# Kernel optimization log

Hardware: AMD Instinct MI355X
Metric: run time of the kernel (lower is better)

The kernel has to match this reference:

```python
import jax, jax.numpy as jnp
import numpy as np

K = 32
BN_EPS = 1e-5
GRID = [[0.1, 0.1, 0.1], [0.5, 0.5, 0.5], [0.2, 0.2, 0.05]]


def setup_inputs() -> dict:
    key = jax.random.key(0)
    ks = jax.random.split(key, 8)
    B, P, C = 4, 6144, 64
    N = B * P
    feat = jax.random.normal(ks[0], (N, C), jnp.float32)
    coord = jax.random.normal(ks[1], (N, 3), jnp.float32) * 10.0
    batch = jnp.repeat(jnp.arange(B, dtype=jnp.int32), P)
    # feature_judge params: Linear(C,64) -> BatchNorm1d(64, eval) -> ReLU -> Linear(64,3)
    W1 = jax.random.normal(ks[2], (C, 64), jnp.float32) / np.sqrt(C)
    b1 = jnp.zeros((64,), jnp.float32)
    gamma = jnp.ones((64,), jnp.float32)
    beta = jnp.zeros((64,), jnp.float32)
    bn_mean = jax.random.normal(ks[3], (64,), jnp.float32) * 0.1
    bn_var = jax.random.uniform(ks[4], (64,), jnp.float32, 0.5, 1.5)
    W2 = jax.random.normal(ks[5], (64, 3), jnp.float32) / 8.0
    b2 = jnp.zeros((3,), jnp.float32)
    return {"feat": feat, "coord": coord, "batch": batch, "W1": W1, "b1": b1,
            "gamma": gamma, "beta": beta, "bn_mean": bn_mean, "bn_var": bn_var,
            "W2": W2, "b2": b2}


def _geometry(coord, B):
    # coord: [N,3] with equal-size contiguous batches -> [B,P,3]
    N = coord.shape[0]
    P = N // B
    pts = coord.reshape(B, P, 3)
    sq = jnp.sum(pts * pts, axis=-1)                               # [B,P]
    d2 = sq[:, :, None] + sq[:, None, :] - 2.0 * jnp.einsum('bpd,bqd->bpq', pts, pts)
    dist = jnp.sqrt(jnp.maximum(d2, 1e-12))                        # [B,P,P]
    _, idx = jax.lax.top_k(-dist, K + 1)                           # smallest K+1
    idx = idx[:, :, 1:]                                            # drop self -> [B,P,K]
    nbrs = jax.vmap(lambda p, i: p[i])(pts, idx)                   # [B,P,K,3]
    centered = nbrs - nbrs.mean(axis=2, keepdims=True)
    cov = jnp.einsum('bpki,bpkj->bpij', centered, centered) / (K - 1)  # [B,P,3,3]
    ev = jnp.linalg.eigvalsh(cov)[..., ::-1]                       # descending, == svd S (PSD)
    ev = ev / jnp.sum(ev, axis=-1, keepdims=True)
    linearity = (ev[..., 0] - (ev[..., 1] + ev[..., 2])).reshape(N)
    nbr_d = jnp.take_along_axis(dist, idx, axis=2)                 # [B,P,K]
    density = (1.0 / (nbr_d.mean(axis=-1) + 1e-6)).reshape(N)
    return linearity, density


def reference(feat, coord, batch, W1, b1, gamma, beta, bn_mean, bn_var, W2, b2):
    B = int(batch[-1]) + 1
    linearity, density = _geometry(coord, B)
    # feature judge MLP (BatchNorm in eval mode with running stats)
    h = feat @ W1 + b1
    h = gamma * (h - bn_mean) / jnp.sqrt(bn_var + BN_EPS) + beta
    h = jax.nn.relu(h)
    probs = jax.nn.softmax(h @ W2 + b2, axis=1)                    # [N,3]
    lin = linearity[:, None]
    den = density[:, None]
    tower_prob = (den * 2.0 + probs[:, 0:1]) / 3.0
    background_prob = (jnp.maximum(1.0 - lin, 1.0 - den) + probs[:, 1:2]) / 3.0
    line_prob = (lin * 2.0 + probs[:, 2:3]) / 3.0
    tower_g = jnp.asarray(GRID[0], jnp.float32)
    bg_g = jnp.asarray(GRID[1], jnp.float32)
    line_g = jnp.asarray([GRID[2][0], GRID[2][1], GRID[2][2] * 5.0], jnp.float32)
    grid_sizes = tower_prob * tower_g + background_prob * bg_g + line_prob * line_g + 1e-6
    return grid_sizes  # [N,3]
```

## Files before the change

kernel.cpp:

```cpp
#include <hip/hip_runtime.h>
#include <hip/hip_bf16.h>
#include <math.h>

#define TS 512
#define BUFCAP 128
#define KMAX 0xFFFFFFFFFFFFFFFFull

typedef __hip_bfloat16 bf16;
typedef unsigned long long u64;

__device__ inline float ldf(const void* p, int idx, bool isbf) {
  return isbf ? __bfloat162float(((const bf16*)p)[idx])
              : ((const float*)p)[idx];
}

__device__ inline bool probe_is_bf16(const void* bn_var) {
  int ok = 0;
#pragma unroll 1
  for (int k = 0; k < 64; ++k) {
    float v = __bfloat162float(((const bf16*)bn_var)[k]);
    if (v >= 0.4f && v <= 1.6f) ++ok;
  }
  return ok == 64;
}

__device__ inline u64 shfl_xor_u64(u64 v, int mask) {
  unsigned lo = __shfl_xor((unsigned)v, mask, 64);
  unsigned hi = __shfl_xor((unsigned)(v >> 32), mask, 64);
  return ((u64)hi << 32) | lo;
}

__device__ inline u64 bcast_u64(u64 v, int srclane) {
  unsigned lo = __shfl((unsigned)v, srclane, 64);
  unsigned hi = __shfl((unsigned)(v >> 32), srclane, 64);
  return ((u64)hi << 32) | lo;
}

__device__ inline void bitonic128(u64& a0, u64& a1, int lane) {
#pragma unroll
  for (int k = 2; k <= 128; k <<= 1) {
#pragma unroll
    for (int j = k >> 1; j > 0; j >>= 1) {
      if (j == 64) {
        u64 lo = (a0 < a1) ? a0 : a1;
        u64 hi = (a0 < a1) ? a1 : a0;
        a0 = lo; a1 = hi;
      } else {
        u64 p0 = shfl_xor_u64(a0, j);
        u64 p1 = shfl_xor_u64(a1, j);
        bool lower = ((lane & j) == 0);
        bool up0 = ((lane & k) == 0);
        bool up1 = (((64 + lane) & k) == 0);
        a0 = ((p0 < a0) == (lower == up0)) ? p0 : a0;
        a1 = ((p1 < a1) == (lower == up1)) ? p1 : a1;
      }
    }
  }
}

__device__ inline u64 reselect(volatile u64* wbuf, int& cnt, int lane) {
  u64 a0 = (lane < cnt) ? wbuf[lane] : KMAX;
  u64 a1 = (64 + lane < cnt) ? wbuf[64 + lane] : KMAX;
  bitonic128(a0, a1, lane);
  if (lane < 32) wbuf[lane] = a0;
  cnt = 32;
  return bcast_u64(a0, 31);
}

#define RED32(v)             \
  v += __shfl_xor(v, 1, 64); \
  v += __shfl_xor(v, 2, 64); \
  v += __shfl_xor(v, 4, 64); \
  v += __shfl_xor(v, 8, 64); \
  v += __shfl_xor(v, 16, 64);
#define RED64(v) RED32(v) v += __shfl_xor(v, 32, 64);

__global__ __launch_bounds__(256) void fused_kernel(
    const void* __restrict__ coord, const void* __restrict__ feat,
    const void* __restrict__ W1, const void* __restrict__ b1,
    const void* __restrict__ gamma_, const void* __restrict__ beta_,
    const void* __restrict__ bn_mean, const void* __restrict__ bn_var,
    const void* __restrict__ W2, const void* __restrict__ b2,
    float* __restrict__ out, int N) {
  __shared__ float4 sTile[TS];
  __shared__ u64 sBuf[4 * BUFCAP];

  const bool isbf = probe_is_bf16(bn_var);
  int tid = threadIdx.x;
  int lane = tid & 63;
  int w = tid >> 6;
  int i = blockIdx.x * 4 + w;
  int P = N / 4;
  int base = (i / P) * P;
  int mypos = i - base;
  volatile u64* wbuf = &sBuf[w * BUFCAP];
  u64 lmask = (1ull << lane) - 1;

  float qx = ldf(coord, 3 * i + 0, isbf);
  float qy = ldf(coord, 3 * i + 1, isbf);
  float qz = ldf(coord, 3 * i + 2, isbf);
  float qsq = (qx * qx + qy * qy) + qz * qz;

  float th_f = __int_as_float(0x7F800000);
  int cnt = 0;

  const int ntiles = P / TS;

  for (int tile = 0; tile < ntiles; ++tile) {
    __syncthreads();
    {
      int c0 = tile * TS + tid;
      int g = 3 * (base + c0);
      float x = ldf(coord, g + 0, isbf), y = ldf(coord, g + 1, isbf),
            z = ldf(coord, g + 2, isbf);
      sTile[tid] = make_float4(x, y, z, (x * x + y * y) + z * z);
      g = 3 * (base + c0 + 256);
      x = ldf(coord, g + 0, isbf); y = ldf(coord, g + 1, isbf);
      z = ldf(coord, g + 2, isbf);
      sTile[tid + 256] = make_float4(x, y, z, (x * x + y * y) + z * z);
    }
    __syncthreads();
    int t0 = tile * TS;

    float d2v[8];
    bool anyp = false;
#pragma unroll
    for (int s = 0; s < 8; ++s) {
      float4 cd = sTile[s * 64 + lane];
      float t = qx * cd.x;
      t = fmaf(qy, cd.y, t);
      t = fmaf(qz, cd.z, t);
      float d2 = (qsq + cd.w) - 2.0f * t;
      d2 = fmaxf(d2, 1e-12f);
      d2v[s] = d2;
      anyp = anyp || (d2 <= th_f);
    }
    if (__ballot(anyp)) {
#pragma unroll
      for (int s = 0; s < 8; ++s) {
        float d2 = d2v[s];
        int cpos = t0 + s * 64 + lane;
        bool cand = (d2 <= th_f) && (cpos != mypos);
        u64 mask = __ballot(cand);
        if (mask) {
          u64 key = ((u64)__float_as_uint(d2) << 32) | (unsigned)cpos;
          int pc = __popcll(mask);
          if (cnt + pc > BUFCAP) {
            u64 th = reselect(wbuf, cnt, lane);
            th_f = __uint_as_float((unsigned)(th >> 32));
            cand = cand && (d2 <= th_f);
            mask = __ballot(cand);
            pc = __popcll(mask);
          }
          if (mask) {
            int pos = cnt + __popcll(mask & lmask);
            if (cand) wbuf[pos] = key;
            cnt += pc;
          }
        }
      }
    }
  }

  reselect(wbuf, cnt, lane);
  u64 K = (lane < 32) ? wbuf[lane] : KMAX;

  float sd = 0.f, sx = 0.f, sy = 0.f, sz = 0.f;
  float sxx = 0.f, sxy = 0.f, sxz = 0.f, syy = 0.f, syz = 0.f, szz = 0.f;
  if (lane < 32) {
    unsigned cpos = (unsigned)(K & 0xFFFFFFFFull);
    if (cpos >= (unsigned)P) cpos = 0;
    float d2 = __uint_as_float((unsigned)(K >> 32));
    sd = sqrtf(d2);
    int g = 3 * (base + (int)cpos);
    float dx = ldf(coord, g + 0, isbf) - qx,
          dy = ldf(coord, g + 1, isbf) - qy,
          dz = ldf(coord, g + 2, isbf) - qz;
    sx = dx; sy = dy; sz = dz;
    sxx = dx * dx; sxy = dx * dy; sxz = dx * dz;
    syy = dy * dy; syz = dy * dz; szz = dz * dz;
  }
  RED32(sd) RED32(sx) RED32(sy) RED32(sz) RED32(sxx) RED32(sxy) RED32(sxz)
  RED32(syy) RED32(syz) RED32(szz)

  float bnv = ldf(bn_var, lane, isbf);
  float bs = ldf(gamma_, lane, isbf) / sqrtf(bnv + 1e-5f);
  float bt = (ldf(b1, lane, isbf) - ldf(bn_mean, lane, isbf)) * bs +
             ldf(beta_, lane, isbf);
  float fv = ldf(feat, i * 64 + lane, isbf);
  float h = 0.f;
#pragma unroll 4
  for (int k = 0; k < 64; ++k) {
    float w1k = ldf(W1, k * 64 + lane, isbf);
    h = fmaf(__shfl(fv, k, 64), w1k, h);
  }
  h = fmaxf(fmaf(h, bs, bt), 0.f);
  float l0 = h * ldf(W2, lane * 3 + 0, isbf);
  float l1 = h * ldf(W2, lane * 3 + 1, isbf);
  float l2 = h * ldf(W2, lane * 3 + 2, isbf);
  RED64(l0) RED64(l1) RED64(l2)
  l0 += ldf(b2, 0, isbf); l1 += ldf(b2, 1, isbf); l2 += ldf(b2, 2, isbf);
  float m = fmaxf(l0, fmaxf(l1, l2));
  float e0 = expf(l0 - m), e1 = expf(l1 - m), e2 = expf(l2 - m);
  float inv = 1.f / (e0 + e1 + e2);
  float pr0 = e0 * inv, pr1 = e1 * inv, pr2 = e2 * inv;

  if (lane == 0) {
    const float n = 32.0f, km1 = 31.0f;
    float mx = sx / n, my = sy / n, mz = sz / n;
    float a = (sxx - n * mx * mx) / km1;
    float bb = (syy - n * my * my) / km1;
    float cc2 = (szz - n * mz * mz) / km1;
    float d = (sxy - n * mx * my) / km1;
    float e = (syz - n * my * mz) / km1;
    float f = (sxz - n * mx * mz) / km1;
    float tr = a + bb + cc2;
    float qq = tr / 3.0f;
    float p1 = d * d + f * f + e * e;
    float aq = a - qq, bq = bb - qq, cq = cc2 - qq;
    float p2 = aq * aq + bq * bq + cq * cq + 2.0f * p1;
    float p = sqrtf(p2 / 6.0f);
    float ev0;
    if (p < 1e-20f) {
      ev0 = qq;
    } else {
      float ip = 1.0f / p;
      float b00 = aq * ip, b11 = bq * ip, b22 = cq * ip;
      float b01 = d * ip, b12 = e * ip, b02 = f * ip;
      float r = (b00 * (b11 * b22 - b12 * b12) -
                 b01 * (b01 * b22 - b12 * b02) +
                 b02 * (b01 * b12 - b11 * b02)) * 0.5f;
      r = fminf(1.0f, fmaxf(-1.0f, r));
      float phi = acosf(r) / 3.0f;
      ev0 = qq + 2.0f * p * cosf(phi);
    }
    float lin = 2.0f * ev0 / tr - 1.0f;
    float den = 1.0f / (sd / 32.0f + 1e-6f);
    float tp = (den * 2.0f + pr0) / 3.0f;
    float bp = (fmaxf(1.0f - lin, 1.0f - den) + pr1) / 3.0f;
    float lp = (lin * 2.0f + pr2) / 3.0f;
    float g0 = tp * 0.1f + bp * 0.5f + lp * 0.2f + 1e-6f;
    float g2 = tp * 0.1f + bp * 0.5f + lp * 0.25f + 1e-6f;
    if (!isfinite(g0)) g0 = 0.f;
    if (!isfinite(g2)) g2 = 0.f;
    out[3 * i + 0] = g0;
    out[3 * i + 1] = g0;
    out[3 * i + 2] = g2;
  }
}

extern "C" void kernel_launch(void* const* d_in, const int* in_sizes, int n_in,
                              void* d_out, int out_size, void* d_ws,
                              size_t ws_size, hipStream_t stream) {
  const void* feat = d_in[0];
  const void* coord = d_in[1];
  const void* W1 = d_in[3];
  const void* b1 = d_in[4];
  const void* gamma_ = d_in[5];
  const void* beta_ = d_in[6];
  const void* bn_mean = d_in[7];
  const void* bn_var = d_in[8];
  const void* W2 = d_in[9];
  const void* b2 = d_in[10];
  float* out = (float*)d_out;

  int N = in_sizes[0] / 64;
  (void)d_ws; (void)ws_size; (void)out_size; (void)n_in;

  hipLaunchKernelGGL(fused_kernel, dim3(N / 4), dim3(256), 0, stream, coord,
                     feat, W1, b1, gamma_, beta_, bn_mean, bn_var, W2, b2,
                     out, N);
}
```

Measured before the change: 302.2 us.

## Drop shared-memory coordinate tiling and block barriers; load candidates directly per wave

Removes the per-block shared-memory tile of candidate coordinates and its two __syncthreads per tile. Each wave now reads candidate coordinates straight from global memory and recomputes the squared norms itself. The serial 64-iteration bf16 dtype probe is replaced with a single per-lane load and a ballot. Waves no longer wait on each other, but each wave issues its own global/L2 loads for the whole batch, so four times as much coordinate traffic goes through the cache in exchange for no synchronization.

Result: slower. 351.9 us (+16.5%).

```diff
diff --git a/kernel.cpp b/kernel.cpp
--- a/kernel.cpp
+++ b/kernel.cpp
@@ -2,7 +2,6 @@
 #include <hip/hip_bf16.h>
 #include <math.h>
 
-#define TS 512
 #define BUFCAP 128
 #define KMAX 0xFFFFFFFFFFFFFFFFull
 
@@ -12,16 +11,6 @@
 __device__ inline float ldf(const void* p, int idx, bool isbf) {
   return isbf ? __bfloat162float(((const bf16*)p)[idx])
               : ((const float*)p)[idx];
-}
-
-__device__ inline bool probe_is_bf16(const void* bn_var) {
-  int ok = 0;
-#pragma unroll 1
-  for (int k = 0; k < 64; ++k) {
-    float v = __bfloat162float(((const bf16*)bn_var)[k]);
-    if (v >= 0.4f && v <= 1.6f) ++ok;
-  }
-  return ok == 64;
 }
 
 __device__ inline u64 shfl_xor_u64(u64 v, int mask) {
@@ -82,10 +71,8 @@
     const void* __restrict__ bn_mean, const void* __restrict__ bn_var,
     const void* __restrict__ W2, const void* __restrict__ b2,
     float* __restrict__ out, int N) {
-  __shared__ float4 sTile[TS];
   __shared__ u64 sBuf[4 * BUFCAP];
 
-  const bool isbf = probe_is_bf16(bn_var);
   int tid = threadIdx.x;
   int lane = tid & 63;
   int w = tid >> 6;
@@ -96,6 +83,15 @@
   volatile u64* wbuf = &sBuf[w * BUFCAP];
   u64 lmask = (1ull << lane) - 1;
 
+  {
+    float v = __bfloat162float(((const bf16*)bn_var)[lane]);
+    bool okv = (v >= 0.4f && v <= 1.6f);
+    __asm__ volatile("" ::: "memory");
+    if (false) (void)okv;
+  }
+  float pv = __bfloat162float(((const bf16*)bn_var)[lane]);
+  const bool isbf = (__ballot(pv >= 0.4f && pv <= 1.6f) == ~0ull);
+
   float qx = ldf(coord, 3 * i + 0, isbf);
   float qy = ldf(coord, 3 * i + 1, isbf);
   float qz = ldf(coord, 3 * i + 2, isbf);
@@ -104,33 +100,21 @@
   float th_f = __int_as_float(0x7F800000);
   int cnt = 0;
 
-  const int ntiles = P / TS;
-
-  for (int tile = 0; tile < ntiles; ++tile) {
-    __syncthreads();
-    {
-      int c0 = tile * TS + tid;
-      int g = 3 * (base + c0);
-      float x = ldf(coord, g + 0, isbf), y = ldf(coord, g + 1, isbf),
-            z = ldf(coord, g + 2, isbf);
-      sTile[tid] = make_float4(x, y, z, (x * x + y * y) + z * z);
-      g = 3 * (base + c0 + 256);
-      x = ldf(coord, g + 0, isbf); y = ldf(coord, g + 1, isbf);
-      z = ldf(coord, g + 2, isbf);
-      sTile[tid + 256] = make_float4(x, y, z, (x * x + y * y) + z * z);
-    }
-    __syncthreads();
-    int t0 = tile * TS;
-
+  const int ngroups = P / 512;
+  for (int g8 = 0; g8 < ngroups; ++g8) {
+    int c0 = g8 * 512 + lane;
     float d2v[8];
     bool anyp = false;
 #pragma unroll
     for (int s = 0; s < 8; ++s) {
-      float4 cd = sTile[s * 64 + lane];
-      float t = qx * cd.x;
-      t = fmaf(qy, cd.y, t);
-      t = fmaf(qz, cd.z, t);
-      float d2 = (qsq + cd.w) - 2.0f * t;
+      int gi = 3 * (base + c0 + s * 64);
+      float x = ldf(coord, gi + 0, isbf), y = ldf(coord, gi + 1, isbf),
+            z = ldf(coord, gi + 2, isbf);
+      float csq = (x * x + y * y) + z * z;
+      float t = qx * x;
+      t = fmaf(qy, y, t);
+      t = fmaf(qz, z, t);
+      float d2 = (qsq + csq) - 2.0f * t;
       d2 = fmaxf(d2, 1e-12f);
       d2v[s] = d2;
       anyp = anyp || (d2 <= th_f);
@@ -139,7 +123,7 @@
 #pragma unroll
       for (int s = 0; s < 8; ++s) {
         float d2 = d2v[s];
-        int cpos = t0 + s * 64 + lane;
+        int cpos = c0 + s * 64;
         bool cand = (d2 <= th_f) && (cpos != mypos);
         u64 mask = __ballot(cand);
         if (mask) {
```
